# Kernel optimization log

Measured on AMD Instinct MI355X. Metric: run time of the kernel, lower is better.

Reference implementation:

```python
import jax, jax.numpy as jnp
import numpy as np

NUM_FREQS = 6

def posenc(x, num_freqs):
    freqs = (2.0 ** jnp.arange(num_freqs)).astype(x.dtype)  # [F]
    ang = x[..., None] * freqs                               # [N, D, F]
    enc = jnp.concatenate([jnp.sin(ang), jnp.cos(ang)], axis=-1)  # [N, D, 2F]
    return enc.reshape(x.shape[0], -1)

def setup_inputs() -> dict:
    key = jax.random.key(0)
    k1, k2, k3 = jax.random.split(key, 3)
    N, D, C = 200000, 6, 256
    E = D * 2 * NUM_FREQS  # 72
    X = jax.random.normal(k1, (N, D), dtype=jnp.float32)
    linear_mappings = jax.random.normal(k2, (3 * C, E), dtype=jnp.float32) * 0.05
    centroids = jax.random.normal(k3, (C, 3), dtype=jnp.float32)
    return {"X": X, "linear_mappings": linear_mappings, "centroids": centroids}

def reference(X, linear_mappings, centroids):
    N = X.shape[0]
    encoded_X = posenc(X, NUM_FREQS)                         # [N, E]
    rgb_clusters = encoded_X @ linear_mappings.T             # [N, 3C]
    rgb_clusters = rgb_clusters.reshape(N, -1, 3)            # [N, C, 3]
    # scores = centroids @ X[:, :3].T  -> softmax over clusters per point
    scores = X[:, :3] @ centroids.T                          # [N, C] (== scores.T in torch code)
    attention_weights = jax.nn.softmax(scores, axis=-1)      # [N, C]
    # torch does diagonal(attn @ rgb_clusters).T == per-row contraction:
    rgb = jnp.einsum('nc,ncd->nd', attention_weights, rgb_clusters)  # [N, 3]
    return rgb
```

## Files before the change

### kernel.cpp

```cpp
#include <hip/hip_runtime.h>
#include <math.h>


#define NCLUST   256
#define M_BLK    128
#define THREADS  256
#define NTILES   15
#define BG_BYTES (NTILES * 8 * 64 * 16)
#define ET_STRIDE 264

typedef __attribute__((ext_vector_type(8))) short bfrag_t;
typedef __attribute__((ext_vector_type(4))) float cfrag_t;
typedef __attribute__((ext_vector_type(4))) unsigned int uifrag_t;

static __device__ __forceinline__ unsigned short f2bf1(float f) {
    return __builtin_bit_cast(unsigned short, (__bf16)f);
}
static __device__ __forceinline__ unsigned int f2bf2(float lo, float hi) {
    return (unsigned int)f2bf1(lo) | ((unsigned int)f2bf1(hi) << 16);
}
static __device__ __forceinline__ float bf2f(unsigned short s) {
    return __uint_as_float(((unsigned int)s) << 16);
}
static __device__ __forceinline__ void glds16(const void* g, void* l) {
    __builtin_amdgcn_global_load_lds(
        (const __attribute__((address_space(1))) unsigned int*)g,
        (__attribute__((address_space(3))) unsigned int*)l, 16, 0, 0);
}

__global__ void prep_kernel(const float* __restrict__ W, uint4* __restrict__ Bg) {
    const int u = blockIdx.x * 256 + threadIdx.x;
    if (u >= NTILES * 8 * 64) return;
    const int lane = u & 63, ks = (u >> 6) & 7, tile = u >> 9;
    const int ln = lane & 15, q = lane >> 4;
    const int jp = tile * 16 + ln;
    const int d  = jp / 80;
    const int e  = jp - d * 80;
    const int c0 = ks * 32 + q * 8;
    unsigned int w[4] = {0u, 0u, 0u, 0u};
    if (e < 72) {
#pragma unroll
        for (int i = 0; i < 4; ++i) {
            float f0 = W[((c0 + 2 * i)     * 3 + d) * 72 + e];
            float f1 = W[((c0 + 2 * i + 1) * 3 + d) * 72 + e];
            w[i] = f2bf2(f0, f1);
        }
    }
    Bg[u] = make_uint4(w[0], w[1], w[2], w[3]);
}

__global__ __launch_bounds__(THREADS, 2) void rgb_attn_mfma(
    const float* __restrict__ X,
    const float* __restrict__ cent,
    const void* __restrict__ Bg,
    float* __restrict__ out, int N)
{
    __shared__ __align__(16) unsigned char encT[80 * ET_STRIDE];
    __shared__ __align__(16) unsigned char Bbuf[2][8192];

    const int tid  = threadIdx.x;
    const int lane = tid & 63;
    const int wv   = tid >> 6;
    const int q    = lane >> 4;
    const int ln   = lane & 15;

#pragma unroll
    for (int i = 0; i < 2; ++i) {
        const int u = i * 256 + wv * 64 + lane;
        glds16((const char*)Bg + u * 16, (char*)Bbuf[0] + u * 16);
    }

    {
        const int pt  = tid & 127;
        const int h   = tid >> 7;
        const int gpt = blockIdx.x * M_BLK + pt;
        const int gp  = (gpt < N) ? gpt : (N - 1);
        unsigned char* colp = encT + pt * 2;
#pragma unroll
        for (int k = 0; k < 3; ++k) {
            const int dd = 3 * h + k;
            const float xv = X[gp * 6 + dd];
            float s[6], c[6];
            __sincosf(xv, &s[0], &c[0]);
#pragma unroll
            for (int f = 1; f < 6; ++f) {
                s[f] = 2.0f * s[f-1] * c[f-1];
                c[f] = 1.0f - 2.0f * s[f-1] * s[f-1];
            }
#pragma unroll
            for (int f = 0; f < 6; ++f) {
                *(unsigned short*)(colp + (dd*12 + f)     * ET_STRIDE) = f2bf1(s[f]);
                *(unsigned short*)(colp + (dd*12 + 6 + f) * ET_STRIDE) = f2bf1(c[f]);
            }
        }
        *(uint2*)(encT + (72 + (tid >> 5)) * ET_STRIDE + (tid & 31) * 8) = make_uint2(0u, 0u);
    }

    uifrag_t afrag[2][8];
    float dA = 0.0f, dB = 0.0f;
    {
        const int pm0 = (2 * wv) * 16 + ln;
        const int g0a = blockIdx.x * M_BLK + pm0;
        const int g0  = (g0a < N) ? g0a : (N - 1);
        const int g1a = g0a + 16;
        const int g1  = (g1a < N) ? g1a : (N - 1);
        const float2 xy0 = *(const float2*)(X + g0 * 6);
        const float  z0  = X[g0 * 6 + 2];
        const float2 xy1 = *(const float2*)(X + g1 * 6);
        const float  z1  = X[g1 * 6 + 2];
        const float4* c4base = (const float4*)cent;
#pragma unroll
        for (int g = 0; g < 8; ++g) {
            const float4* c4 = c4base + (6 * q + 24 * g);
            const float4 v0 = c4[0], v1 = c4[1], v2 = c4[2];
            const float4 v3 = c4[3], v4 = c4[4], v5 = c4[5];
            float cx[8], cy[8], cz[8];
            cx[0]=v0.x; cy[0]=v0.y; cz[0]=v0.z;
            cx[1]=v0.w; cy[1]=v1.x; cz[1]=v1.y;
            cx[2]=v1.z; cy[2]=v1.w; cz[2]=v2.x;
            cx[3]=v2.y; cy[3]=v2.z; cz[3]=v2.w;
            cx[4]=v3.x; cy[4]=v3.y; cz[4]=v3.z;
            cx[5]=v3.w; cy[5]=v4.x; cz[5]=v4.y;
            cx[6]=v4.z; cy[6]=v4.w; cz[6]=v5.x;
            cx[7]=v5.y; cy[7]=v5.z; cz[7]=v5.w;
            float ea[8], eb[8];
#pragma unroll
            for (int j = 0; j < 8; ++j) {
                ea[j] = __expf(fmaf(xy0.x, cx[j], fmaf(xy0.y, cy[j], z0 * cz[j])));
                eb[j] = __expf(fmaf(xy1.x, cx[j], fmaf(xy1.y, cy[j], z1 * cz[j])));
                dA += ea[j]; dB += eb[j];
            }
#pragma unroll
            for (int w = 0; w < 4; ++w) {
                afrag[0][g][w] = f2bf2(ea[2*w], ea[2*w+1]);
                afrag[1][g][w] = f2bf2(eb[2*w], eb[2*w+1]);
            }
        }
    }

    __syncthreads();

    float part[3][2][4] = {};
#pragma unroll
    for (int t = 0; t < NTILES; ++t) {
        if (t) __syncthreads();
        if (t < NTILES - 1) {
#pragma unroll
            for (int i = 0; i < 2; ++i) {
                const int u = i * 256 + wv * 64 + lane;
                glds16((const char*)Bg + ((t + 1) * 512 + u) * 16,
                       (char*)Bbuf[(t + 1) & 1] + u * 16);
            }
        }
        cfrag_t a0 = {0.f,0.f,0.f,0.f}, a1 = {0.f,0.f,0.f,0.f};
#pragma unroll
        for (int ks = 0; ks < 8; ++ks) {
            const bfrag_t b = *(const bfrag_t*)(Bbuf[t & 1] + (ks * 64 + lane) * 16);
            a0 = __builtin_amdgcn_mfma_f32_16x16x32_bf16(
                     __builtin_bit_cast(bfrag_t, afrag[0][ks]), b, a0, 0, 0, 0);
            a1 = __builtin_amdgcn_mfma_f32_16x16x32_bf16(
                     __builtin_bit_cast(bfrag_t, afrag[1][ks]), b, a1, 0, 0, 0);
        }
        const int d  = t / 5;
        const int er = (t % 5) * 16 + ln;
#pragma unroll
        for (int mt = 0; mt < 2; ++mt) {
            const ushort4 ev = *(const ushort4*)(encT + er * ET_STRIDE
                                   + ((2 * wv + mt) * 16 + q * 4) * 2);
            const cfrag_t a = mt ? a1 : a0;
            part[d][mt][0] = fmaf(a[0], bf2f(ev.x), part[d][mt][0]);
            part[d][mt][1] = fmaf(a[1], bf2f(ev.y), part[d][mt][1]);
            part[d][mt][2] = fmaf(a[2], bf2f(ev.z), part[d][mt][2]);
            part[d][mt][3] = fmaf(a[3], bf2f(ev.w), part[d][mt][3]);
        }
    }

#pragma unroll
    for (int mask = 1; mask <= 8; mask <<= 1)
#pragma unroll
        for (int d = 0; d < 3; ++d)
#pragma unroll
            for (int mt = 0; mt < 2; ++mt)
#pragma unroll
                for (int r = 0; r < 4; ++r)
                    part[d][mt][r] += __shfl_xor(part[d][mt][r], mask, 64);

    dA += __shfl_xor(dA, 16, 64); dA += __shfl_xor(dA, 32, 64);
    dB += __shfl_xor(dB, 16, 64); dB += __shfl_xor(dB, 32, 64);
    const float iA = 1.0f / dA;
    const float iB = 1.0f / dB;
    float invr[2][4];
#pragma unroll
    for (int r = 0; r < 4; ++r) {
        invr[0][r] = __shfl(iA, q * 4 + r, 64);
        invr[1][r] = __shfl(iB, q * 4 + r, 64);
    }

    if (ln == 0) {
#pragma unroll
        for (int mt = 0; mt < 2; ++mt)
#pragma unroll
            for (int r = 0; r < 4; ++r) {
                const int pm = (2 * wv + mt) * 16 + q * 4 + r;
                const int g  = blockIdx.x * M_BLK + pm;
                if (g < N) {
                    out[g*3+0] = part[0][mt][r] * invr[mt][r];
                    out[g*3+1] = part[1][mt][r] * invr[mt][r];
                    out[g*3+2] = part[2][mt][r] * invr[mt][r];
                }
            }
    }
}

__global__ __launch_bounds__(256) void rgb_attn_fallback(
    const float* __restrict__ X, const float* __restrict__ W,
    const float* __restrict__ cent, float* __restrict__ out, int N)
{
    const int n = blockIdx.x * 256 + threadIdx.x;
    const bool valid = (n < N);
    float x[6];
#pragma unroll
    for (int k = 0; k < 6; ++k) x[k] = valid ? X[n * 6 + k] : 0.0f;
    float enc[72];
#pragma unroll
    for (int d = 0; d < 6; ++d)
#pragma unroll
        for (int f = 0; f < 6; ++f) {
            float s, c;
            __sincosf(x[d] * (float)(1 << f), &s, &c);
            enc[d*12+f] = s; enc[d*12+6+f] = c;
        }
    float acc0 = 0, acc1 = 0, acc2 = 0, denom = 0;
#pragma unroll 1
    for (int c = 0; c < NCLUST; ++c) {
        float s = fmaf(x[0], cent[c*3], fmaf(x[1], cent[c*3+1], x[2]*cent[c*3+2]));
        float ew = __expf(s);
        const float* w = W + c * 216;
        float d0 = 0, d1 = 0, d2 = 0;
#pragma unroll
        for (int e = 0; e < 72; ++e) {
            float ee = enc[e];
            d0 = fmaf(ee, w[e], d0);
            d1 = fmaf(ee, w[72 + e], d1);
            d2 = fmaf(ee, w[144 + e], d2);
        }
        denom += ew;
        acc0 = fmaf(ew, d0, acc0); acc1 = fmaf(ew, d1, acc1); acc2 = fmaf(ew, d2, acc2);
    }
    if (valid) {
        float inv = 1.0f / denom;
        out[n*3+0] = acc0*inv; out[n*3+1] = acc1*inv; out[n*3+2] = acc2*inv;
    }
}

extern "C" void kernel_launch(void* const* d_in, const int* in_sizes, int n_in,
                              void* d_out, int out_size, void* d_ws, size_t ws_size,
                              hipStream_t stream)
{
    const float* X    = (const float*)d_in[0];
    const float* W    = (const float*)d_in[1];
    const float* cent = (const float*)d_in[2];
    float* out = (float*)d_out;
    const int N = in_sizes[0] / 6;

    if (ws_size >= (size_t)BG_BYTES) {
        uint4* Bg = (uint4*)d_ws;
        prep_kernel<<<(NTILES * 8 * 64 + 255) / 256, 256, 0, stream>>>(W, Bg);
        const int blocks = (N + M_BLK - 1) / M_BLK;
        rgb_attn_mfma<<<blocks, THREADS, 0, stream>>>(X, cent, (const void*)Bg, out, N);
    } else {
        rgb_attn_fallback<<<(N + 255) / 256, 256, 0, stream>>>(X, W, cent, out, N);
    }
}
```

Measured before the change: 116.6 us.

## Use single-wave blocks and read weight fragments directly from global/L2

Shrinks each block to one wavefront handling 32 points and removes the shared-memory double buffer for the weight tiles. Each lane now loads its B fragments straight from global memory, relying on L1/L2 caching of the small prep buffer, and all __syncthreads barriers go away. The per-block encoding tile shrinks to match. This trades block-level barriers and LDS staging for more global load traffic and many more small blocks.

New measurement: 158.7 us. 1.36x slower.

```diff
diff --git a/kernel.cpp b/kernel.cpp
--- a/kernel.cpp
+++ b/kernel.cpp
@@ -3,11 +3,11 @@
 
 
 #define NCLUST   256
-#define M_BLK    128
-#define THREADS  256
+#define M_BLK    32
+#define THREADS  64
 #define NTILES   15
 #define BG_BYTES (NTILES * 8 * 64 * 16)
-#define ET_STRIDE 264
+#define ET_STRIDE 72
 
 typedef __attribute__((ext_vector_type(8))) short bfrag_t;
 typedef __attribute__((ext_vector_type(4))) float cfrag_t;
@@ -21,11 +21,6 @@
 }
 static __device__ __forceinline__ float bf2f(unsigned short s) {
     return __uint_as_float(((unsigned int)s) << 16);
-}
-static __device__ __forceinline__ void glds16(const void* g, void* l) {
-    __builtin_amdgcn_global_load_lds(
-        (const __attribute__((address_space(1))) unsigned int*)g,
-        (__attribute__((address_space(3))) unsigned int*)l, 16, 0, 0);
 }
 
 __global__ void prep_kernel(const float* __restrict__ W, uint4* __restrict__ Bg) {
@@ -49,30 +44,21 @@
     Bg[u] = make_uint4(w[0], w[1], w[2], w[3]);
 }
 
-__global__ __launch_bounds__(THREADS, 2) void rgb_attn_mfma(
+__global__ __launch_bounds__(THREADS, 3) void rgb_attn_mfma(
     const float* __restrict__ X,
     const float* __restrict__ cent,
     const void* __restrict__ Bg,
     float* __restrict__ out, int N)
 {
     __shared__ __align__(16) unsigned char encT[80 * ET_STRIDE];
-    __shared__ __align__(16) unsigned char Bbuf[2][8192];
-
-    const int tid  = threadIdx.x;
-    const int lane = tid & 63;
-    const int wv   = tid >> 6;
+
+    const int lane = threadIdx.x;
     const int q    = lane >> 4;
     const int ln   = lane & 15;
 
-#pragma unroll
-    for (int i = 0; i < 2; ++i) {
-        const int u = i * 256 + wv * 64 + lane;
-        glds16((const char*)Bg + u * 16, (char*)Bbuf[0] + u * 16);
-    }
-
     {
-        const int pt  = tid & 127;
-        const int h   = tid >> 7;
+        const int pt  = lane & 31;
+        const int h   = lane >> 5;
         const int gpt = blockIdx.x * M_BLK + pt;
         const int gp  = (gpt < N) ? gpt : (N - 1);
         unsigned char* colp = encT + pt * 2;
@@ -93,14 +79,13 @@
                 *(unsigned short*)(colp + (dd*12 + 6 + f) * ET_STRIDE) = f2bf1(c[f]);
             }
         }
-        *(uint2*)(encT + (72 + (tid >> 5)) * ET_STRIDE + (tid & 31) * 8) = make_uint2(0u, 0u);
+        *(uint2*)(encT + (72 + (lane >> 3)) * ET_STRIDE + (lane & 7) * 8) = make_uint2(0u, 0u);
     }
 
     uifrag_t afrag[2][8];
     float dA = 0.0f, dB = 0.0f;
     {
-        const int pm0 = (2 * wv) * 16 + ln;
-        const int g0a = blockIdx.x * M_BLK + pm0;
+        const int g0a = blockIdx.x * M_BLK + ln;
         const int g0  = (g0a < N) ? g0a : (N - 1);
         const int g1a = g0a + 16;
         const int g1  = (g1a < N) ? g1a : (N - 1);
@@ -138,35 +123,27 @@
         }
     }
 
-    __syncthreads();
-
+    const char* Bgc = (const char*)Bg + lane * 16;
     float part[3][2][4] = {};
 #pragma unroll
     for (int t = 0; t < NTILES; ++t) {
-        if (t) __syncthreads();
-        if (t < NTILES - 1) {
-#pragma unroll
-            for (int i = 0; i < 2; ++i) {
-                const int u = i * 256 + wv * 64 + lane;
-                glds16((const char*)Bg + ((t + 1) * 512 + u) * 16,
-                       (char*)Bbuf[(t + 1) & 1] + u * 16);
-            }
-        }
+        bfrag_t b[8];
+#pragma unroll
+        for (int ks = 0; ks < 8; ++ks)
+            b[ks] = *(const bfrag_t*)(Bgc + (t * 8 + ks) * 1024);
         cfrag_t a0 = {0.f,0.f,0.f,0.f}, a1 = {0.f,0.f,0.f,0.f};
 #pragma unroll
         for (int ks = 0; ks < 8; ++ks) {
-            const bfrag_t b = *(const bfrag_t*)(Bbuf[t & 1] + (ks * 64 + lane) * 16);
             a0 = __builtin_amdgcn_mfma_f32_16x16x32_bf16(
-                     __builtin_bit_cast(bfrag_t, afrag[0][ks]), b, a0, 0, 0, 0);
+                     __builtin_bit_cast(bfrag_t, afrag[0][ks]), b[ks], a0, 0, 0, 0);
             a1 = __builtin_amdgcn_mfma_f32_16x16x32_bf16(
-                     __builtin_bit_cast(bfrag_t, afrag[1][ks]), b, a1, 0, 0, 0);
+                     __builtin_bit_cast(bfrag_t, afrag[1][ks]), b[ks], a1, 0, 0, 0);
         }
         const int d  = t / 5;
         const int er = (t % 5) * 16 + ln;
 #pragma unroll
         for (int mt = 0; mt < 2; ++mt) {
-            const ushort4 ev = *(const ushort4*)(encT + er * ET_STRIDE
-                                   + ((2 * wv + mt) * 16 + q * 4) * 2);
+            const ushort4 ev = *(const ushort4*)(encT + er * ET_STRIDE + mt * 32 + q * 8);
             const cfrag_t a = mt ? a1 : a0;
             part[d][mt][0] = fmaf(a[0], bf2f(ev.x), part[d][mt][0]);
             part[d][mt][1] = fmaf(a[1], bf2f(ev.y), part[d][mt][1]);
@@ -201,7 +178,7 @@
         for (int mt = 0; mt < 2; ++mt)
 #pragma unroll
             for (int r = 0; r < 4; ++r) {
-                const int pm = (2 * wv + mt) * 16 + q * 4 + r;
+                const int pm = mt * 16 + q * 4 + r;
                 const int g  = blockIdx.x * M_BLK + pm;
                 if (g < N) {
                     out[g*3+0] = part[0][mt][r] * invr[mt][r];
```
